# Kernel optimization log

Hardware: AMD Instinct MI355X
Metric: run time of the kernel (lower is better)

The kernel has to match this reference:

```python
import jax, jax.numpy as jnp
import numpy as np

B, S, D = 256, 512, 128
H1, H2 = 256, 512


def setup_inputs() -> dict:
    key = jax.random.key(0)
    ks = jax.random.split(key, 13)
    s = lambda k, shape, scale=0.05: jax.random.normal(k, shape, dtype=jnp.float32) * scale
    return {
        "x": jax.random.normal(ks[0], (B, S, D), dtype=jnp.float32),
        "conv_w": s(ks[1], (H1, D)),
        "conv_b": s(ks[2], (H1,)),
        "w_ih": s(ks[3], (4 * H2, H1)),
        "b_ih": s(ks[4], (4 * H2,)),
        "w_hh": s(ks[5], (4 * H2, H2)),
        "b_hh": s(ks[6], (4 * H2,)),
        "h0": s(ks[7], (B, H2)),
        "c0": s(ks[8], (B, H2)),
        "fc1_w": s(ks[9], (H2, H2)),
        "fc1_b": s(ks[10], (H2,)),
        "fc2_w": s(ks[11], (1, H2)),
        "fc2_b": s(ks[12], (1,)),
    }


def reference(x, conv_w, conv_b, w_ih, b_ih, w_hh, b_hh, h0, c0,
              fc1_w, fc1_b, fc2_w, fc2_b):
    # Conv1d with kernel_size=1 == pointwise linear over feature dim
    embed = jnp.einsum('bsd,hd->bsh', x, conv_w) + conv_b  # [B,S,H1]

    def step(carry, e_t):
        h, c = carry
        # PyTorch LSTMCell: gates in order i, f, g, o
        gates = e_t @ w_ih.T + b_ih + h @ w_hh.T + b_hh  # [B,4H2]
        i, f, g, o = jnp.split(gates, 4, axis=-1)
        i = jax.nn.sigmoid(i)
        f = jax.nn.sigmoid(f)
        g = jnp.tanh(g)
        o = jax.nn.sigmoid(o)
        c = f * c + i * g
        h = o * jnp.tanh(c)
        return (h, c), h

    _, hs = jax.lax.scan(step, (h0, c0), jnp.swapaxes(embed, 0, 1))  # hs: [S,B,H2]
    pooled = hs.sum(axis=0)  # sum over sequence -> [B,H2]
    dec = jax.nn.relu(pooled @ fc1_w.T + fc1_b)
    v = (dec @ fc2_w.T + fc2_b).squeeze(-1)  # [B]
    return v
```

## Files before the change

kernel.cpp:

```cpp
#include <hip/hip_runtime.h>
#include <hip/hip_cooperative_groups.h>


typedef __attribute__((ext_vector_type(8))) short s16x8;
typedef __attribute__((ext_vector_type(4))) float f32x4;
typedef __attribute__((ext_vector_type(2))) float f32x2;

#define B_   256
#define S_   512
#define D_   128
#define H1_  256
#define H2_  512
#define G4_  2048
#define K_   640

__device__ __forceinline__ unsigned short f2bf(float f) {
  union { float f; unsigned u; } v; v.f = f;
  unsigned r = v.u + 0x7FFFu + ((v.u >> 16) & 1u);
  return (unsigned short)(r >> 16);
}
__device__ __forceinline__ float sigm(float x) { return 1.f / (1.f + __expf(-x)); }
__device__ __forceinline__ float tanh_(float x) { return 1.f - 2.f / (__expf(2.f * x) + 1.f); }

__device__ __forceinline__ s16x8 ld_cohx8(const unsigned short* p) {
  s16x8 d;
  asm volatile("global_load_dwordx4 %0, %1, off sc0 sc1" : "=v"(d) : "v"(p));
  return d;
}
__device__ __forceinline__ void st_coh_u32(unsigned* p, unsigned v) {
  asm volatile("global_store_dword %0, %1, off sc0 sc1" :: "v"(p), "v"(v) : "memory");
}
__device__ __forceinline__ unsigned ld_coh_u32(const unsigned* p) {
  unsigned d;
  asm volatile("global_load_dword %0, %1, off sc0 sc1\n\ts_waitcnt vmcnt(0)"
               : "=v"(d) : "v"(p) : "memory");
  return d;
}
__device__ __forceinline__ void vm_drain() {
  asm volatile("s_waitcnt vmcnt(0)" ::: "memory");
  __builtin_amdgcn_sched_barrier(0);
}

__global__ void prep_kernel(const float* __restrict__ conv_w, const float* __restrict__ conv_b,
                            const float* __restrict__ w_ih,   const float* __restrict__ b_ih,
                            const float* __restrict__ w_hh,   const float* __restrict__ b_hh,
                            unsigned short* __restrict__ Wc,  float* __restrict__ bias,
                            unsigned* __restrict__ flags) {
  const int np = blockIdx.x;
  const int c = np >> 5, r5 = np & 31;
  const int blk = r5 >> 4, q = (r5 >> 2) & 3, g = r5 & 3;
  const int j = c * 8 + 2 * q + blk;
  const int n = g * H2_ + j;
  const int tid = threadIdx.x;

  if (np == 0) { flags[tid] = 0; flags[tid + 128] = 0; }

  __shared__ float wrow[H1_];
  __shared__ float red[128];
  wrow[tid]       = w_ih[(size_t)n * H1_ + tid];
  wrow[tid + 128] = w_ih[(size_t)n * H1_ + tid + 128];
  __syncthreads();

  float acc = 0.f;
  for (int h1 = 0; h1 < H1_; ++h1)
    acc += wrow[h1] * conv_w[(size_t)h1 * D_ + tid];
  Wc[(size_t)np * K_ + tid] = f2bf(acc);

  #pragma unroll
  for (int r = 0; r < 4; ++r)
    Wc[(size_t)np * K_ + 128 + tid + r * 128] = f2bf(w_hh[(size_t)n * H2_ + tid + r * 128]);

  float p = wrow[tid] * conv_b[tid] + wrow[tid + 128] * conv_b[tid + 128];
  red[tid] = p;
  __syncthreads();
  for (int s = 64; s > 0; s >>= 1) {
    if (tid < s) red[tid] += red[tid + s];
    __syncthreads();
  }
  if (tid == 0) bias[4 * j + g] = red[0] + b_ih[n] + b_hh[n];
}

__global__ __launch_bounds__(256, 1) void lstm_kernel(
    const float* __restrict__ x, const float* __restrict__ h0,
    const float* __restrict__ c0, const unsigned short* __restrict__ Wc,
    const float* __restrict__ bias, unsigned short* __restrict__ h_bf,
    float* __restrict__ pooled, unsigned* __restrict__ flags) {
  const int wg = blockIdx.x;
  const int mg = wg & 15;
  const int ng = wg >> 4;
  const int tid = threadIdx.x;
  const int wv = tid >> 6;
  const int lane = tid & 63;

  __shared__ unsigned short Alds[16 * K_];

  const int n0 = ng * 128 + wv * 32;
  s16x8 bfrag0[20], bfrag1[20];
  {
    const int bn0 = n0 + (lane & 15);
    const int bk = (lane >> 4) * 8;
    #pragma unroll
    for (int kk = 0; kk < 20; ++kk) {
      bfrag0[kk] = *(const s16x8*)(Wc + (size_t)bn0 * K_ + kk * 32 + bk);
      bfrag1[kk] = *(const s16x8*)(Wc + (size_t)(bn0 + 16) * K_ + kk * 32 + bk);
    }
  }
  #pragma unroll
  for (int kk = 0; kk < 20; ++kk)
    asm volatile("" : "+v"(bfrag0[kk]), "+v"(bfrag1[kk]));

  const int b_own = mg * 16 + (lane & 15);
  const int j0 = ng * 32 + wv * 8 + 2 * (lane >> 4);
  const f32x4 brg0 = *(const f32x4*)(bias + 4 * j0);
  const f32x4 brg1 = *(const f32x4*)(bias + 4 * (j0 + 1));
  f32x2 c_reg = *(const f32x2*)(c0 + (size_t)b_own * H2_ + j0);
  f32x2 pool_acc = {0.f, 0.f};

  const int sr = tid >> 4, sct = tid & 15;
  const int b_st = mg * 16 + sr;
  const unsigned row_base = sr * (K_ * 2);
  const unsigned swz = (unsigned)((sr & 7) << 4);
  const unsigned swz_x = (row_base + sct * 16) ^ swz;

  const int ar = lane & 15;
  const int ahi = lane >> 4;
  unsigned* fgrp = flags + mg * 16;

  {
    const float* xp = x + ((size_t)b_st * S_) * D_ + sct * 8;
    f32x4 v0 = *(const f32x4*)xp;
    f32x4 v1 = *(const f32x4*)(xp + 4);
    s16x8 pk;
    pk[0] = (short)f2bf(v0[0]); pk[1] = (short)f2bf(v0[1]);
    pk[2] = (short)f2bf(v0[2]); pk[3] = (short)f2bf(v0[3]);
    pk[4] = (short)f2bf(v1[0]); pk[5] = (short)f2bf(v1[1]);
    pk[6] = (short)f2bf(v1[2]); pk[7] = (short)f2bf(v1[3]);
    *(s16x8*)((char*)Alds + swz_x) = pk;
  }

  #pragma unroll 1
  for (int t = 0; t < S_; ++t) {
    unsigned short* hout = h_bf + ((t + 1) & 1) * (B_ * H2_);

    if (t == 0) {
      const float* hp = h0 + (size_t)b_st * H2_ + sct * 32;
      #pragma unroll
      for (int q = 0; q < 4; ++q) {
        f32x4 a = *(const f32x4*)(hp + q * 8);
        f32x4 b = *(const f32x4*)(hp + q * 8 + 4);
        s16x8 pk;
        pk[0] = (short)f2bf(a[0]); pk[1] = (short)f2bf(a[1]);
        pk[2] = (short)f2bf(a[2]); pk[3] = (short)f2bf(a[3]);
        pk[4] = (short)f2bf(b[0]); pk[5] = (short)f2bf(b[1]);
        pk[6] = (short)f2bf(b[2]); pk[7] = (short)f2bf(b[3]);
        unsigned byte = row_base + 256 + sct * 64 + q * 16;
        *(s16x8*)((char*)Alds + (byte ^ swz)) = pk;
      }
    } else {
      const unsigned short* hin = h_bf + (t & 1) * (B_ * H2_);
      const unsigned short* hrow = hin + (size_t)b_st * H2_ + sct * 32;
      s16x8 hv0 = ld_cohx8(hrow);
      s16x8 hv1 = ld_cohx8(hrow + 8);
      s16x8 hv2 = ld_cohx8(hrow + 16);
      s16x8 hv3 = ld_cohx8(hrow + 24);
      vm_drain();
      unsigned byte = row_base + 256 + sct * 64;
      *(s16x8*)((char*)Alds + ((byte     ) ^ swz)) = hv0;
      *(s16x8*)((char*)Alds + ((byte + 16) ^ swz)) = hv1;
      *(s16x8*)((char*)Alds + ((byte + 32) ^ swz)) = hv2;
      *(s16x8*)((char*)Alds + ((byte + 48) ^ swz)) = hv3;
    }
    f32x4 vx0, vx1;
    if (t < S_ - 1) {
      const float* xp = x + ((size_t)b_st * S_ + (t + 1)) * D_ + sct * 8;
      vx0 = *(const f32x4*)xp;
      vx1 = *(const f32x4*)(xp + 4);
    }
    __syncthreads();

    f32x4 acc0 = {0.f, 0.f, 0.f, 0.f};
    f32x4 acc1 = {0.f, 0.f, 0.f, 0.f};
    #pragma unroll
    for (int kk = 0; kk < 20; ++kk) {
      unsigned byte = (unsigned)(ar * (K_ * 2) + kk * 64 + ahi * 16);
      s16x8 af = *(const s16x8*)((const char*)Alds + (byte ^ ((ar & 7) << 4)));
      acc0 = __builtin_amdgcn_mfma_f32_16x16x32_bf16(bfrag0[kk], af, acc0, 0, 0, 0);
      acc1 = __builtin_amdgcn_mfma_f32_16x16x32_bf16(bfrag1[kk], af, acc1, 0, 0, 0);
    }

    {
      float iA = sigm(acc0[0] + brg0[0]);
      float fA = sigm(acc0[1] + brg0[1]);
      float gA = tanh_(acc0[2] + brg0[2]);
      float oA = sigm(acc0[3] + brg0[3]);
      c_reg[0] = fA * c_reg[0] + iA * gA;
      float hA = oA * tanh_(c_reg[0]);
      pool_acc[0] += hA;
      float iB = sigm(acc1[0] + brg1[0]);
      float fB = sigm(acc1[1] + brg1[1]);
      float gB = tanh_(acc1[2] + brg1[2]);
      float oB = sigm(acc1[3] + brg1[3]);
      c_reg[1] = fB * c_reg[1] + iB * gB;
      float hB = oB * tanh_(c_reg[1]);
      pool_acc[1] += hB;
      if (t < S_ - 1) {
        unsigned packed = (unsigned)f2bf(hA) | ((unsigned)f2bf(hB) << 16);
        st_coh_u32((unsigned*)(hout + (size_t)b_own * H2_ + j0), packed);
      }
    }

    if (t < S_ - 1) {
      s16x8 pk;
      pk[0] = (short)f2bf(vx0[0]); pk[1] = (short)f2bf(vx0[1]);
      pk[2] = (short)f2bf(vx0[2]); pk[3] = (short)f2bf(vx0[3]);
      pk[4] = (short)f2bf(vx1[0]); pk[5] = (short)f2bf(vx1[1]);
      pk[6] = (short)f2bf(vx1[2]); pk[7] = (short)f2bf(vx1[3]);

      vm_drain();
      __syncthreads();
      if (tid == 0) st_coh_u32(fgrp + ng, (unsigned)(t + 1));

      *(s16x8*)((char*)Alds + swz_x) = pk;

      const unsigned tgt = (unsigned)(t + 1);
      const unsigned* fp = fgrp + (lane & 15);
      while (!__all(ld_coh_u32(fp) >= tgt))
        __builtin_amdgcn_s_sleep(1);
    }
  }

  *(f32x2*)(pooled + (size_t)b_own * H2_ + j0) = pool_acc;
}

__global__ void fc_kernel(const float* __restrict__ pooled,
                          const float* __restrict__ fc1_w, const float* __restrict__ fc1_b,
                          const float* __restrict__ fc2_w, const float* __restrict__ fc2_b,
                          float* __restrict__ out) {
  const int b = blockIdx.x;
  const int tid = threadIdx.x;
  __shared__ float prow[H2_];
  __shared__ float dec[H2_];
  __shared__ float red[256];
  prow[tid]       = pooled[(size_t)b * H2_ + tid];
  prow[tid + 256] = pooled[(size_t)b * H2_ + tid + 256];
  __syncthreads();
  #pragma unroll
  for (int e = 0; e < 2; ++e) {
    const int o = tid + e * 256;
    const float* wrow = fc1_w + (size_t)o * H2_;
    float a = fc1_b[o];
    #pragma unroll 8
    for (int k = 0; k < H2_; ++k) a += prow[k] * wrow[k];
    dec[o] = fmaxf(a, 0.f);
  }
  __syncthreads();
  red[tid] = dec[tid] * fc2_w[tid] + dec[tid + 256] * fc2_w[tid + 256];
  __syncthreads();
  for (int s = 128; s > 0; s >>= 1) {
    if (tid < s) red[tid] += red[tid + s];
    __syncthreads();
  }
  if (tid == 0) out[b] = red[0] + fc2_b[0];
}

extern "C" void kernel_launch(void* const* d_in, const int* in_sizes, int n_in,
                              void* d_out, int out_size, void* d_ws, size_t ws_size,
                              hipStream_t stream) {
  const float* x      = (const float*)d_in[0];
  const float* conv_w = (const float*)d_in[1];
  const float* conv_b = (const float*)d_in[2];
  const float* w_ih   = (const float*)d_in[3];
  const float* b_ih   = (const float*)d_in[4];
  const float* w_hh   = (const float*)d_in[5];
  const float* b_hh   = (const float*)d_in[6];
  const float* h0     = (const float*)d_in[7];
  const float* c0     = (const float*)d_in[8];
  const float* fc1_w  = (const float*)d_in[9];
  const float* fc1_b  = (const float*)d_in[10];
  const float* fc2_w  = (const float*)d_in[11];
  const float* fc2_b  = (const float*)d_in[12];
  float* out = (float*)d_out;

  char* ws = (char*)d_ws;
  unsigned short* Wc    = (unsigned short*)(ws);
  float* bias           = (float*)(ws + 2621440);
  unsigned short* h_bf  = (unsigned short*)(ws + 2629632);
  float* pooled         = (float*)(ws + 3153920);
  unsigned* flags       = (unsigned*)(ws + 3678208);

  prep_kernel<<<dim3(G4_), dim3(128), 0, stream>>>(conv_w, conv_b, w_ih, b_ih,
                                                   w_hh, b_hh, Wc, bias, flags);

  void* args[8];
  args[0] = (void*)&x;    args[1] = (void*)&h0;   args[2] = (void*)&c0;
  args[3] = (void*)&Wc;   args[4] = (void*)&bias; args[5] = (void*)&h_bf;
  args[6] = (void*)&pooled; args[7] = (void*)&flags;
  hipLaunchCooperativeKernel((void*)lstm_kernel, dim3(256), dim3(256), args, 0, stream);

  fc_kernel<<<dim3(B_), dim3(256), 0, stream>>>(pooled, fc1_w, fc1_b, fc2_w, fc2_b, out);
}
```

Measured before the change: 1.784 ms.

## Ping-pong two batch halves per workgroup to overlap LSTM sync with compute

Each workgroup now processes two 16-row batch slices (A and B) with separate LDS buffers and flag groups. It computes one half while the other half's hidden-state exchange is in flight, which hides the cross-workgroup flag-wait latency. The grid is halved to 128 workgroups and launched normally instead of cooperatively. The risk is that spin-waiting without a cooperative launch relies on all 128 workgroups being co-resident.

```diff
diff --git a/kernel.cpp b/kernel.cpp
--- a/kernel.cpp
+++ b/kernel.cpp
@@ -1,5 +1,4 @@
 #include <hip/hip_runtime.h>
-#include <hip/hip_cooperative_groups.h>
 
 
 typedef __attribute__((ext_vector_type(8))) short s16x8;
@@ -86,13 +85,13 @@
     const float* __restrict__ bias, unsigned short* __restrict__ h_bf,
     float* __restrict__ pooled, unsigned* __restrict__ flags) {
   const int wg = blockIdx.x;
-  const int mg = wg & 15;
-  const int ng = wg >> 4;
+  const int mg = wg & 7;
+  const int ng = wg >> 3;
   const int tid = threadIdx.x;
   const int wv = tid >> 6;
   const int lane = tid & 63;
 
-  __shared__ unsigned short Alds[16 * K_];
+  __shared__ unsigned short Alds[2][16 * K_];
 
   const int n0 = ng * 128 + wv * 32;
   s16x8 bfrag0[20], bfrag1[20];
@@ -109,127 +108,184 @@
   for (int kk = 0; kk < 20; ++kk)
     asm volatile("" : "+v"(bfrag0[kk]), "+v"(bfrag1[kk]));
 
-  const int b_own = mg * 16 + (lane & 15);
+  const int b_ownA = mg * 16 + (lane & 15);
+  const int b_ownB = 128 + mg * 16 + (lane & 15);
   const int j0 = ng * 32 + wv * 8 + 2 * (lane >> 4);
   const f32x4 brg0 = *(const f32x4*)(bias + 4 * j0);
   const f32x4 brg1 = *(const f32x4*)(bias + 4 * (j0 + 1));
-  f32x2 c_reg = *(const f32x2*)(c0 + (size_t)b_own * H2_ + j0);
-  f32x2 pool_acc = {0.f, 0.f};
+  f32x2 cA = *(const f32x2*)(c0 + (size_t)b_ownA * H2_ + j0);
+  f32x2 cB = *(const f32x2*)(c0 + (size_t)b_ownB * H2_ + j0);
+  f32x2 poolA = {0.f, 0.f}, poolB = {0.f, 0.f};
 
   const int sr = tid >> 4, sct = tid & 15;
-  const int b_st = mg * 16 + sr;
+  const int b_stA = mg * 16 + sr;
+  const int b_stB = 128 + mg * 16 + sr;
   const unsigned row_base = sr * (K_ * 2);
   const unsigned swz = (unsigned)((sr & 7) << 4);
   const unsigned swz_x = (row_base + sct * 16) ^ swz;
 
   const int ar = lane & 15;
   const int ahi = lane >> 4;
-  unsigned* fgrp = flags + mg * 16;
-
-  {
-    const float* xp = x + ((size_t)b_st * S_) * D_ + sct * 8;
-    f32x4 v0 = *(const f32x4*)xp;
-    f32x4 v1 = *(const f32x4*)(xp + 4);
-    s16x8 pk;
-    pk[0] = (short)f2bf(v0[0]); pk[1] = (short)f2bf(v0[1]);
-    pk[2] = (short)f2bf(v0[2]); pk[3] = (short)f2bf(v0[3]);
-    pk[4] = (short)f2bf(v1[0]); pk[5] = (short)f2bf(v1[1]);
-    pk[6] = (short)f2bf(v1[2]); pk[7] = (short)f2bf(v1[3]);
-    *(s16x8*)((char*)Alds + swz_x) = pk;
+  unsigned* fA = flags + mg * 16;
+  unsigned* fB = flags + 128 + mg * 16;
+
+  #pragma unroll
+  for (int s = 0; s < 2; ++s) {
+    const int b_st = s ? b_stB : b_stA;
+    char* lds = (char*)Alds[s];
+    {
+      const float* xp = x + ((size_t)b_st * S_) * D_ + sct * 8;
+      f32x4 v0 = *(const f32x4*)xp;
+      f32x4 v1 = *(const f32x4*)(xp + 4);
+      s16x8 pk;
+      pk[0] = (short)f2bf(v0[0]); pk[1] = (short)f2bf(v0[1]);
+      pk[2] = (short)f2bf(v0[2]); pk[3] = (short)f2bf(v0[3]);
+      pk[4] = (short)f2bf(v1[0]); pk[5] = (short)f2bf(v1[1]);
+      pk[6] = (short)f2bf(v1[2]); pk[7] = (short)f2bf(v1[3]);
+      *(s16x8*)(lds + swz_x) = pk;
+    }
+    const float* hp = h0 + (size_t)b_st * H2_ + sct * 32;
+    #pragma unroll
+    for (int q = 0; q < 4; ++q) {
+      f32x4 a = *(const f32x4*)(hp + q * 8);
+      f32x4 b = *(const f32x4*)(hp + q * 8 + 4);
+      s16x8 pk;
+      pk[0] = (short)f2bf(a[0]); pk[1] = (short)f2bf(a[1]);
+      pk[2] = (short)f2bf(a[2]); pk[3] = (short)f2bf(a[3]);
+      pk[4] = (short)f2bf(b[0]); pk[5] = (short)f2bf(b[1]);
+      pk[6] = (short)f2bf(b[2]); pk[7] = (short)f2bf(b[3]);
+      unsigned byte = row_base + 256 + sct * 64 + q * 16;
+      *(s16x8*)(lds + (byte ^ swz)) = pk;
+    }
   }
 
   #pragma unroll 1
   for (int t = 0; t < S_; ++t) {
     unsigned short* hout = h_bf + ((t + 1) & 1) * (B_ * H2_);
-
-    if (t == 0) {
-      const float* hp = h0 + (size_t)b_st * H2_ + sct * 32;
+    const unsigned short* hin = h_bf + (t & 1) * (B_ * H2_);
+    const bool more = (t < S_ - 1);
+
+    __syncthreads();
+    f32x4 vxa0, vxa1;
+    if (more) {
+      const float* xp = x + ((size_t)b_stA * S_ + (t + 1)) * D_ + sct * 8;
+      vxa0 = *(const f32x4*)xp;
+      vxa1 = *(const f32x4*)(xp + 4);
+    }
+    {
+      f32x4 acc0 = {0.f, 0.f, 0.f, 0.f};
+      f32x4 acc1 = {0.f, 0.f, 0.f, 0.f};
       #pragma unroll
-      for (int q = 0; q < 4; ++q) {
-        f32x4 a = *(const f32x4*)(hp + q * 8);
-        f32x4 b = *(const f32x4*)(hp + q * 8 + 4);
-        s16x8 pk;
-        pk[0] = (short)f2bf(a[0]); pk[1] = (short)f2bf(a[1]);
-        pk[2] = (short)f2bf(a[2]); pk[3] = (short)f2bf(a[3]);
-        pk[4] = (short)f2bf(b[0]); pk[5] = (short)f2bf(b[1]);
-        pk[6] = (short)f2bf(b[2]); pk[7] = (short)f2bf(b[3]);
-        unsigned byte = row_base + 256 + sct * 64 + q * 16;
-        *(s16x8*)((char*)Alds + (byte ^ swz)) = pk;
+      for (int kk = 0; kk < 20; ++kk) {
+        unsigned byte = (unsigned)(ar * (K_ * 2) + kk * 64 + ahi * 16);
+        s16x8 af = *(const s16x8*)((const char*)Alds[0] + (byte ^ ((ar & 7) << 4)));
+        acc0 = __builtin_amdgcn_mfma_f32_16x16x32_bf16(bfrag0[kk], af, acc0, 0, 0, 0);
+        acc1 = __builtin_amdgcn_mfma_f32_16x16x32_bf16(bfrag1[kk], af, acc1, 0, 0, 0);
       }
-    } else {
-      const unsigned short* hin = h_bf + (t & 1) * (B_ * H2_);
-      const unsigned short* hrow = hin + (size_t)b_st * H2_ + sct * 32;
+      float i0 = sigm(acc0[0] + brg0[0]), f0 = sigm(acc0[1] + brg0[1]);
+      float g0 = tanh_(acc0[2] + brg0[2]), o0 = sigm(acc0[3] + brg0[3]);
+      cA[0] = f0 * cA[0] + i0 * g0;
+      float hA0 = o0 * tanh_(cA[0]);  poolA[0] += hA0;
+      float i1 = sigm(acc1[0] + brg1[0]), f1 = sigm(acc1[1] + brg1[1]);
+      float g1 = tanh_(acc1[2] + brg1[2]), o1 = sigm(acc1[3] + brg1[3]);
+      cA[1] = f1 * cA[1] + i1 * g1;
+      float hA1 = o1 * tanh_(cA[1]);  poolA[1] += hA1;
+      if (more) {
+        unsigned packed = (unsigned)f2bf(hA0) | ((unsigned)f2bf(hA1) << 16);
+        st_coh_u32((unsigned*)(hout + (size_t)b_ownA * H2_ + j0), packed);
+      }
+    }
+    if (more) {
+      s16x8 pk;
+      pk[0] = (short)f2bf(vxa0[0]); pk[1] = (short)f2bf(vxa0[1]);
+      pk[2] = (short)f2bf(vxa0[2]); pk[3] = (short)f2bf(vxa0[3]);
+      pk[4] = (short)f2bf(vxa1[0]); pk[5] = (short)f2bf(vxa1[1]);
+      pk[6] = (short)f2bf(vxa1[2]); pk[7] = (short)f2bf(vxa1[3]);
+      vm_drain();
+      __syncthreads();
+      if (tid == 0) st_coh_u32(fA + ng, (unsigned)(t + 1));
+      *(s16x8*)((char*)Alds[0] + swz_x) = pk;
+    }
+
+    if (t > 0) {
+      const unsigned tgt = (unsigned)t;
+      const unsigned* fp = fB + (lane & 15);
+      while (!__all(ld_coh_u32(fp) >= tgt))
+        __builtin_amdgcn_s_sleep(1);
+      const unsigned short* hrow = hin + (size_t)b_stB * H2_ + sct * 32;
       s16x8 hv0 = ld_cohx8(hrow);
       s16x8 hv1 = ld_cohx8(hrow + 8);
       s16x8 hv2 = ld_cohx8(hrow + 16);
       s16x8 hv3 = ld_cohx8(hrow + 24);
       vm_drain();
       unsigned byte = row_base + 256 + sct * 64;
-      *(s16x8*)((char*)Alds + ((byte     ) ^ swz)) = hv0;
-      *(s16x8*)((char*)Alds + ((byte + 16) ^ swz)) = hv1;
-      *(s16x8*)((char*)Alds + ((byte + 32) ^ swz)) = hv2;
-      *(s16x8*)((char*)Alds + ((byte + 48) ^ swz)) = hv3;
-    }
-    f32x4 vx0, vx1;
-    if (t < S_ - 1) {
-      const float* xp = x + ((size_t)b_st * S_ + (t + 1)) * D_ + sct * 8;
-      vx0 = *(const f32x4*)xp;
-      vx1 = *(const f32x4*)(xp + 4);
-    }
+      *(s16x8*)((char*)Alds[1] + ((byte     ) ^ swz)) = hv0;
+      *(s16x8*)((char*)Alds[1] + ((byte + 16) ^ swz)) = hv1;
+      *(s16x8*)((char*)Alds[1] + ((byte + 32) ^ swz)) = hv2;
+      *(s16x8*)((char*)Alds[1] + ((byte + 48) ^ swz)) = hv3;
+    }
+
     __syncthreads();
-
-    f32x4 acc0 = {0.f, 0.f, 0.f, 0.f};
-    f32x4 acc1 = {0.f, 0.f, 0.f, 0.f};
-    #pragma unroll
-    for (int kk = 0; kk < 20; ++kk) {
-      unsigned byte = (unsigned)(ar * (K_ * 2) + kk * 64 + ahi * 16);
-      s16x8 af = *(const s16x8*)((const char*)Alds + (byte ^ ((ar & 7) << 4)));
-      acc0 = __builtin_amdgcn_mfma_f32_16x16x32_bf16(bfrag0[kk], af, acc0, 0, 0, 0);
-      acc1 = __builtin_amdgcn_mfma_f32_16x16x32_bf16(bfrag1[kk], af, acc1, 0, 0, 0);
-    }
-
+    f32x4 vxb0, vxb1;
+    if (more) {
+      const float* xp = x + ((size_t)b_stB * S_ + (t + 1)) * D_ + sct * 8;
+      vxb0 = *(const f32x4*)xp;
+      vxb1 = *(const f32x4*)(xp + 4);
+    }
     {
-      float iA = sigm(acc0[0] + brg0[0]);
-      float fA = sigm(acc0[1] + brg0[1]);
-      float gA = tanh_(acc0[2] + brg0[2]);
-      float oA = sigm(acc0[3] + brg0[3]);
-      c_reg[0] = fA * c_reg[0] + iA * gA;
-      float hA = oA * tanh_(c_reg[0]);
-      pool_acc[0] += hA;
-      float iB = sigm(acc1[0] + brg1[0]);
-      float fB = sigm(acc1[1] + brg1[1]);
-      float gB = tanh_(acc1[2] + brg1[2]);
-      float oB = sigm(acc1[3] + brg1[3]);
-      c_reg[1] = fB * c_reg[1] + iB * gB;
-      float hB = oB * tanh_(c_reg[1]);
-      pool_acc[1] += hB;
-      if (t < S_ - 1) {
-        unsigned packed = (unsigned)f2bf(hA) | ((unsigned)f2bf(hB) << 16);
-        st_coh_u32((unsigned*)(hout + (size_t)b_own * H2_ + j0), packed);
+      f32x4 acc0 = {0.f, 0.f, 0.f, 0.f};
+      f32x4 acc1 = {0.f, 0.f, 0.f, 0.f};
+      #pragma unroll
+      for (int kk = 0; kk < 20; ++kk) {
+        unsigned byte = (unsigned)(ar * (K_ * 2) + kk * 64 + ahi * 16);
+        s16x8 af = *(const s16x8*)((const char*)Alds[1] + (byte ^ ((ar & 7) << 4)));
+        acc0 = __builtin_amdgcn_mfma_f32_16x16x32_bf16(bfrag0[kk], af, acc0, 0, 0, 0);
+        acc1 = __builtin_amdgcn_mfma_f32_16x16x32_bf16(bfrag1[kk], af, acc1, 0, 0, 0);
       }
-    }
-
-    if (t < S_ - 1) {
+      float i0 = sigm(acc0[0] + brg0[0]), f0 = sigm(acc0[1] + brg0[1]);
+      float g0 = tanh_(acc0[2] + brg0[2]), o0 = sigm(acc0[3] + brg0[3]);
+      cB[0] = f0 * cB[0] + i0 * g0;
+      float hB0 = o0 * tanh_(cB[0]);  poolB[0] += hB0;
+      float i1 = sigm(acc1[0] + brg1[0]), f1 = sigm(acc1[1] + brg1[1]);
+      float g1 = tanh_(acc1[2] + brg1[2]), o1 = sigm(acc1[3] + brg1[3]);
+      cB[1] = f1 * cB[1] + i1 * g1;
+      float hB1 = o1 * tanh_(cB[1]);  poolB[1] += hB1;
+      if (more) {
+        unsigned packed = (unsigned)f2bf(hB0) | ((unsigned)f2bf(hB1) << 16);
+        st_coh_u32((unsigned*)(hout + (size_t)b_ownB * H2_ + j0), packed);
+      }
+    }
+    if (more) {
       s16x8 pk;
-      pk[0] = (short)f2bf(vx0[0]); pk[1] = (short)f2bf(vx0[1]);
-      pk[2] = (short)f2bf(vx0[2]); pk[3] = (short)f2bf(vx0[3]);
-      pk[4] = (short)f2bf(vx1[0]); pk[5] = (short)f2bf(vx1[1]);
-      pk[6] = (short)f2bf(vx1[2]); pk[7] = (short)f2bf(vx1[3]);
-
+      pk[0] = (short)f2bf(vxb0[0]); pk[1] = (short)f2bf(vxb0[1]);
+      pk[2] = (short)f2bf(vxb0[2]); pk[3] = (short)f2bf(vxb0[3]);
+      pk[4] = (short)f2bf(vxb1[0]); pk[5] = (short)f2bf(vxb1[1]);
+      pk[6] = (short)f2bf(vxb1[2]); pk[7] = (short)f2bf(vxb1[3]);
       vm_drain();
       __syncthreads();
-      if (tid == 0) st_coh_u32(fgrp + ng, (unsigned)(t + 1));
-
-      *(s16x8*)((char*)Alds + swz_x) = pk;
+      if (tid == 0) st_coh_u32(fB + ng, (unsigned)(t + 1));
+      *(s16x8*)((char*)Alds[1] + swz_x) = pk;
 
       const unsigned tgt = (unsigned)(t + 1);
-      const unsigned* fp = fgrp + (lane & 15);
+      const unsigned* fp = fA + (lane & 15);
       while (!__all(ld_coh_u32(fp) >= tgt))
         __builtin_amdgcn_s_sleep(1);
-    }
-  }
-
-  *(f32x2*)(pooled + (size_t)b_own * H2_ + j0) = pool_acc;
+      const unsigned short* hrow = hout + (size_t)b_stA * H2_ + sct * 32;
+      s16x8 hv0 = ld_cohx8(hrow);
+      s16x8 hv1 = ld_cohx8(hrow + 8);
+      s16x8 hv2 = ld_cohx8(hrow + 16);
+      s16x8 hv3 = ld_cohx8(hrow + 24);
+      vm_drain();
+      unsigned byte = row_base + 256 + sct * 64;
+      *(s16x8*)((char*)Alds[0] + ((byte     ) ^ swz)) = hv0;
+      *(s16x8*)((char*)Alds[0] + ((byte + 16) ^ swz)) = hv1;
+      *(s16x8*)((char*)Alds[0] + ((byte + 32) ^ swz)) = hv2;
+      *(s16x8*)((char*)Alds[0] + ((byte + 48) ^ swz)) = hv3;
+    }
+  }
+
+  *(f32x2*)(pooled + (size_t)b_ownA * H2_ + j0) = poolA;
+  *(f32x2*)(pooled + (size_t)b_ownB * H2_ + j0) = poolB;
 }
 
 __global__ void fc_kernel(const float* __restrict__ pooled,
@@ -291,11 +347,8 @@
   prep_kernel<<<dim3(G4_), dim3(128), 0, stream>>>(conv_w, conv_b, w_ih, b_ih,
                                                    w_hh, b_hh, Wc, bias, flags);
 
-  void* args[8];
-  args[0] = (void*)&x;    args[1] = (void*)&h0;   args[2] = (void*)&c0;
-  args[3] = (void*)&Wc;   args[4] = (void*)&bias; args[5] = (void*)&h_bf;
-  args[6] = (void*)&pooled; args[7] = (void*)&flags;
-  hipLaunchCooperativeKernel((void*)lstm_kernel, dim3(256), dim3(256), args, 0, stream);
+  lstm_kernel<<<dim3(128), dim3(256), 0, stream>>>(x, h0, c0, Wc, bias,
+                                                   h_bf, pooled, flags);
 
   fc_kernel<<<dim3(B_), dim3(256), 0, stream>>>(pooled, fc1_w, fc1_b, fc2_w, fc2_b, out);
 }
```

After: 2.862 ms. 60.4% more time.
